# Performance work log

Hardware: AMD Instinct MI355X
Metric: run time of the kernel (lower is better)

## Reference

```python
import jax, jax.numpy as jnp
import numpy as np
from jax import lax

EPS = 1e-5
K = 7
G = 4


def _dwconv_bn(x, w, g, b, m, v):
    # depthwise 3x3, pad 1, then BN (eval mode with running stats)
    C = x.shape[1]
    y = lax.conv_general_dilated(x, w, (1, 1), [(1, 1), (1, 1)],
                                 feature_group_count=C,
                                 dimension_numbers=('NCHW', 'OIHW', 'NCHW'))
    scale = (g / jnp.sqrt(v + EPS))[None, :, None, None]
    return (y - m[None, :, None, None]) * scale + b[None, :, None, None]


def _proj(t, pw1, pb1, pw2, pb2):
    # 1x1 conv -> GELU(exact) -> 1x1 conv, on small spatial maps
    h = jnp.einsum('bchw,oc->bohw', t, pw1) + pb1[None, :, None, None]
    h = jax.nn.gelu(h, approximate=False)
    return jnp.einsum('bchw,oc->bohw', h, pw2) + pb2[None, :, None, None]


def setup_inputs() -> dict:
    key = jax.random.key(0)
    ks = jax.random.split(key, 17)
    B, C, H, W = 16, 256, 56, 56
    r = C // 4
    inp = {
        'x1': jax.random.normal(ks[0], (B, C, H, W), jnp.float32),
        'dw1_w': jax.random.normal(ks[1], (C, 1, 3, 3), jnp.float32) * 0.1,
        'dw1_g': jax.random.uniform(ks[2], (C,), jnp.float32, 0.5, 1.5),
        'dw1_b': jax.random.normal(ks[3], (C,), jnp.float32) * 0.1,
        'dw1_m': jax.random.normal(ks[4], (C,), jnp.float32) * 0.1,
        'dw1_v': jax.random.uniform(ks[5], (C,), jnp.float32, 0.5, 1.5),
        'dw2_w': jax.random.normal(ks[6], (C, 1, 3, 3), jnp.float32) * 0.1,
        'dw2_g': jax.random.uniform(ks[7], (C,), jnp.float32, 0.5, 1.5),
        'dw2_b': jax.random.normal(ks[8], (C,), jnp.float32) * 0.1,
        'dw2_m': jax.random.normal(ks[9], (C,), jnp.float32) * 0.1,
        'dw2_v': jax.random.uniform(ks[10], (C,), jnp.float32, 0.5, 1.5),
        'weight1': jax.random.normal(ks[11], (G, C, K, K), jnp.float32) * 0.02,
        'bias1': jax.random.normal(ks[12], (G, C), jnp.float32) * 0.02,
        'pw1': jax.random.normal(ks[13], (r, C), jnp.float32) * 0.05,
        'pb1': jax.random.normal(ks[14], (r,), jnp.float32) * 0.05,
        'pw2': jax.random.normal(ks[15], (C * G, r), jnp.float32) * 0.05,
        'pb2': jax.random.normal(ks[16], (C * G,), jnp.float32) * 0.05,
    }
    return inp


def reference(x1, dw1_w, dw1_g, dw1_b, dw1_m, dw1_v,
              dw2_w, dw2_g, dw2_b, dw2_m, dw2_v,
              weight1, bias1, pw1, pb1, pw2, pb2):
    B, C, H, W = x1.shape
    # gated fuse: relu6(dw1(x)) * dw2(x)
    a = jnp.clip(_dwconv_bn(x1, dw1_w, dw1_g, dw1_b, dw1_m, dw1_v), 0.0, 6.0)
    x_fuse = a * _dwconv_bn(x1, dw2_w, dw2_g, dw2_b, dw2_m, dw2_v)

    # adaptive avg pool to (K,K): H,W multiples of K -> uniform block means
    pooled = x_fuse.reshape(B, C, K, H // K, K, W // K).mean(axis=(3, 5))

    # dynamic kernel: proj -> softmax over groups -> weighted sum of weight1
    scale1 = _proj(pooled, pw1, pb1, pw2, pb2).reshape(B, G, C, K, K)
    scale1 = jax.nn.softmax(scale1, axis=1)
    w_dyn = jnp.sum(scale1 * weight1[None], axis=1)  # [B, C, K, K]

    # dynamic bias
    mean_x = x_fuse.mean(axis=(-2, -1), keepdims=True)  # [B, C, 1, 1]
    sb = _proj(mean_x, pw1, pb1, pw2, pb2).reshape(B, G, C)
    sb = jax.nn.softmax(sb, axis=1)
    b_dyn = jnp.sum(sb * bias1[None], axis=1)  # [B, C]

    # per-sample depthwise conv with dynamic weights
    pad = K // 2

    def per_sample(xi, wi):  # xi [C,H,W], wi [C,K,K]
        y = lax.conv_general_dilated(xi[None], wi[:, None], (1, 1),
                                     [(pad, pad), (pad, pad)],
                                     feature_group_count=C,
                                     dimension_numbers=('NCHW', 'OIHW', 'NCHW'))
        return y[0]

    out = jax.vmap(per_sample)(x_fuse, w_dyn)  # [B, C, H, W]
    return out + b_dyn[:, :, None, None]
```

## Files before the change

### kernel.cpp

```cpp
#include <hip/hip_runtime.h>
#include <math.h>

#define BATCH 16
#define CH 256
#define HW 56
#define NPIX (HW*HW)

__device__ __forceinline__ void fuse_tile(
    const float* __restrict__ plane, int ty, int tx,
    const float w1[9], const float w2[9],
    float sc1, float be1, float sc2, float be2,
    float res[4][4])
{
    const int oy = 4 * ty;
    float y1a[4][4], y2a[4][4];
    #pragma unroll
    for (int a = 0; a < 4; a++)
        #pragma unroll
        for (int e = 0; e < 4; e++) { y1a[a][e] = 0.f; y2a[a][e] = 0.f; }

    #pragma unroll
    for (int iy = 0; iy < 6; iy++) {
        const int r    = oy - 1 + iy;
        const bool rok = (r >= 0) && (r < 56);
        const int rc   = rok ? r : 0;
        float rb[12];
        #pragma unroll
        for (int k = 0; k < 3; k++) {
            const int cx  = tx - 1 + k;
            const bool cv = (cx >= 0) && (cx < 14);
            const int cc2 = cv ? cx : 0;
            const bool ok = rok && cv;
            float4 v = *(const float4*)(plane + rc*56 + 4*cc2);
            rb[4*k+0] = ok ? v.x : 0.f;
            rb[4*k+1] = ok ? v.y : 0.f;
            rb[4*k+2] = ok ? v.z : 0.f;
            rb[4*k+3] = ok ? v.w : 0.f;
        }
        #pragma unroll
        for (int tyy = 0; tyy < 4; tyy++) {
            const int ky = iy - tyy;
            if (ky >= 0 && ky < 3) {
                #pragma unroll
                for (int e = 0; e < 4; e++)
                    #pragma unroll
                    for (int dj = 0; dj < 3; dj++) {
                        float xv = rb[3 + e + dj];
                        y1a[tyy][e] += xv * w1[ky*3+dj];
                        y2a[tyy][e] += xv * w2[ky*3+dj];
                    }
            }
        }
    }
    #pragma unroll
    for (int tyy = 0; tyy < 4; tyy++)
        #pragma unroll
        for (int e = 0; e < 4; e++) {
            float y1 = y1a[tyy][e] * sc1 + be1;
            float y2 = y2a[tyy][e] * sc2 + be2;
            float a = fminf(fmaxf(y1, 0.f), 6.f);
            res[tyy][e] = a * y2;
        }
}

__global__ __launch_bounds__(256) void k1_pool(
    const float* __restrict__ x1,
    const float* __restrict__ dw1w, const float* __restrict__ g1, const float* __restrict__ b1,
    const float* __restrict__ m1, const float* __restrict__ v1,
    const float* __restrict__ dw2w, const float* __restrict__ g2, const float* __restrict__ b2,
    const float* __restrict__ m2, const float* __restrict__ v2,
    float* __restrict__ pooled)
{
    const int bc = blockIdx.x;
    const int c  = bc & 255;
    const int b  = bc >> 8;
    const int t  = threadIdx.x;

    __shared__ float part[196];

    float w1[9], w2[9];
    #pragma unroll
    for (int k = 0; k < 9; k++) { w1[k] = dw1w[c*9+k]; w2[k] = dw2w[c*9+k]; }
    const float sc1 = g1[c] * rsqrtf(v1[c] + 1e-5f);
    const float be1 = b1[c] - m1[c] * sc1;
    const float sc2 = g2[c] * rsqrtf(v2[c] + 1e-5f);
    const float be2 = b2[c] - m2[c] * sc2;

    if (t < 196) {
        const int ty = t / 14, tx = t - ty * 14;
        float res[4][4];
        fuse_tile(x1 + (size_t)bc * NPIX, ty, tx, w1, w2, sc1, be1, sc2, be2, res);
        float s = 0.f;
        #pragma unroll
        for (int a = 0; a < 4; a++)
            #pragma unroll
            for (int e = 0; e < 4; e++) s += res[a][e];
        part[t] = s;
    }
    __syncthreads();
    if (t < 49) {
        int ph = t / 7, pw = t - ph * 7;
        float s = part[(2*ph  )*14 + 2*pw] + part[(2*ph  )*14 + 2*pw + 1]
                + part[(2*ph+1)*14 + 2*pw] + part[(2*ph+1)*14 + 2*pw + 1];
        pooled[((size_t)(b * 50 + t)) * 256 + c] = s * (1.f/64.f);
    }
}

__global__ __launch_bounds__(256) void k2a(
    const float* __restrict__ pooled,
    const float* __restrict__ pw1, const float* __restrict__ pb1,
    float* __restrict__ h)
{
    const int blk = blockIdx.x;
    const int b = blk / 50, p = blk - b * 50;
    const int t = threadIdx.x;

    __shared__ __attribute__((aligned(16))) float xs[272];

    const float* base = pooled + (size_t)b * 50 * 256;
    float v;
    if (p < 49) {
        v = base[p * 256 + t];
    } else {
        float s = 0.f;
        #pragma unroll 7
        for (int q = 0; q < 49; q++) s += base[q * 256 + t];
        v = s * (1.f/49.f);
    }
    xs[t + 4*(t>>6)] = v;
    __syncthreads();

    const int o = t >> 2, part = t & 3;
    const float4* w4 = (const float4*)(pw1 + o*256 + part*64);
    const float4* x4 = (const float4*)(xs + part*68);
    float acc = 0.f;
    #pragma unroll
    for (int i = 0; i < 16; i++) {
        float4 w = w4[i];
        float4 x = x4[i];
        acc += w.x*x.x + w.y*x.y + w.z*x.z + w.w*x.w;
    }
    acc += __shfl_xor(acc, 1);
    acc += __shfl_xor(acc, 2);
    if (part == 0) {
        float zv = acc + pb1[o];
        h[((size_t)b * 50 + p) * 64 + o] = 0.5f * zv * (1.f + erff(zv * 0.70710678118654752f));
    }
}

__global__ __launch_bounds__(256) void k2b(
    const float* __restrict__ h, const float* __restrict__ pw2, const float* __restrict__ pb2,
    const float* __restrict__ weight1, const float* __restrict__ bias1,
    float* __restrict__ w_dyn,
    float* __restrict__ b_dyn)
{
    const int b   = blockIdx.x;
    const int cch = blockIdx.y;
    const int t   = threadIdx.x;
    const int c_base = cch * 16;

    __shared__ float ht[64*52];
    __shared__ __attribute__((aligned(16))) float wg[16*64*4];

    const float* hp = h + (size_t)b * 50 * 64;
    for (int idx = t; idx < 800; idx += 256) {
        const int p = idx >> 4, k4 = idx & 15;
        float4 v = ((const float4*)(hp + p * 64))[k4];
        ht[(4*k4+0)*52 + p] = v.x;
        ht[(4*k4+1)*52 + p] = v.y;
        ht[(4*k4+2)*52 + p] = v.z;
        ht[(4*k4+3)*52 + p] = v.w;
    }
    for (int idx = t; idx < 1024; idx += 256) {
        const int r = idx >> 4, k4 = idx & 15;
        const int g = r >> 4, cl = r & 15;
        const int o2 = (g << 8) + c_base + cl;
        float4 v = ((const float4*)(pw2 + (size_t)o2 * 64))[k4];
        wg[((cl*64) + 4*k4+0)*4 + g] = v.x;
        wg[((cl*64) + 4*k4+1)*4 + g] = v.y;
        wg[((cl*64) + 4*k4+2)*4 + g] = v.z;
        wg[((cl*64) + 4*k4+3)*4 + g] = v.w;
    }
    __syncthreads();

    for (int idx = t; idx < 800; idx += 256) {
        const int cl = idx / 50, p = idx - cl * 50;
        const int c  = c_base + cl;
        float s0 = pb2[c], s1 = pb2[256 + c], s2 = pb2[512 + c], s3 = pb2[768 + c];
        const float4* wv = (const float4*)wg + cl * 64;
        #pragma unroll
        for (int k = 0; k < 64; k++) {
            const float x = ht[k*52 + p];
            const float4 w = wv[k];
            s0 += x * w.x; s1 += x * w.y; s2 += x * w.z; s3 += x * w.w;
        }
        float mx = fmaxf(fmaxf(s0, s1), fmaxf(s2, s3));
        float e0 = expf(s0-mx), e1 = expf(s1-mx), e2 = expf(s2-mx), e3 = expf(s3-mx);
        float inv = 1.f / (e0+e1+e2+e3);
        e0 *= inv; e1 *= inv; e2 *= inv; e3 *= inv;
        if (p < 49) {
            float wvv = e0*weight1[(0*256+c)*49+p] + e1*weight1[(1*256+c)*49+p]
                      + e2*weight1[(2*256+c)*49+p] + e3*weight1[(3*256+c)*49+p];
            w_dyn[((size_t)b*256 + c)*49 + p] = wvv;
        } else {
            b_dyn[b*256 + c] = e0*bias1[c] + e1*bias1[256+c] + e2*bias1[512+c] + e3*bias1[768+c];
        }
    }
}

#define S3 68
__global__ __launch_bounds__(256) void k3_dyn(
    const float* __restrict__ x1,
    const float* __restrict__ dw1w, const float* __restrict__ g1, const float* __restrict__ b1,
    const float* __restrict__ m1, const float* __restrict__ v1,
    const float* __restrict__ dw2w, const float* __restrict__ g2, const float* __restrict__ b2,
    const float* __restrict__ m2, const float* __restrict__ v2,
    const float* __restrict__ w_dyn, const float* __restrict__ b_dyn,
    float* __restrict__ out)
{
    const int bc = blockIdx.x;
    const int c  = bc & 255;
    const int t  = threadIdx.x;
    __shared__ __attribute__((aligned(16))) float halo[62*S3];

    float w1[9], w2[9];
    #pragma unroll
    for (int k = 0; k < 9; k++) { w1[k] = dw1w[c*9+k]; w2[k] = dw2w[c*9+k]; }
    const float sc1 = g1[c] * rsqrtf(v1[c] + 1e-5f);
    const float be1 = b1[c] - m1[c] * sc1;
    const float sc2 = g2[c] * rsqrtf(v2[c] + 1e-5f);
    const float be2 = b2[c] - m2[c] * sc2;
    float wk[49];
    const float* wp = w_dyn + (size_t)bc * 49;
    #pragma unroll
    for (int k = 0; k < 49; k++) wk[k] = wp[k];
    const float bias = b_dyn[bc];

    {
        float4 z = make_float4(0.f, 0.f, 0.f, 0.f);
        float4* h4 = (float4*)halo;
        for (int i = t; i < 62*S3/4; i += 256) h4[i] = z;
    }
    __syncthreads();

    const int ty = t / 14, tx = t - ty * 14;
    if (t < 196) {
        float res[4][4];
        fuse_tile(x1 + (size_t)bc * NPIX, ty, tx, w1, w2, sc1, be1, sc2, be2, res);
        #pragma unroll
        for (int tyy = 0; tyy < 4; tyy++) {
            float4 r4; r4.x=res[tyy][0]; r4.y=res[tyy][1]; r4.z=res[tyy][2]; r4.w=res[tyy][3];
            *(float4*)&halo[(4*ty + tyy + 3)*S3 + 4 + 4*tx] = r4;
        }
    }
    __syncthreads();

    if (t < 196) {
        const int oy = ty * 4, ox = tx * 4;
        float acc[4][4];
        #pragma unroll
        for (int a = 0; a < 4; a++)
            #pragma unroll
            for (int bb = 0; bb < 4; bb++) acc[a][bb] = bias;

        #pragma unroll
        for (int iy = 0; iy < 10; iy++) {
            const float* hr = &halo[(oy+iy)*S3 + ox];
            float4 a = *(const float4*)hr;
            float4 b = *(const float4*)(hr + 4);
            float4 cc = *(const float4*)(hr + 8);
            float row[12];
            row[0]=a.x; row[1]=a.y; row[2]=a.z; row[3]=a.w;
            row[4]=b.x; row[5]=b.y; row[6]=b.z; row[7]=b.w;
            row[8]=cc.x; row[9]=cc.y; row[10]=cc.z; row[11]=cc.w;
            #pragma unroll
            for (int tyy = 0; tyy < 4; tyy++) {
                const int ky = iy - tyy;
                if (ky >= 0 && ky < 7) {
                    #pragma unroll
                    for (int txx = 0; txx < 4; txx++)
                        #pragma unroll
                        for (int kx = 0; kx < 7; kx++)
                            acc[tyy][txx] += row[1+txx+kx] * wk[ky*7+kx];
                }
            }
        }
        float* op = out + (size_t)bc * NPIX;
        #pragma unroll
        for (int tyy = 0; tyy < 4; tyy++) {
            float4 r4; r4.x = acc[tyy][0]; r4.y = acc[tyy][1]; r4.z = acc[tyy][2]; r4.w = acc[tyy][3];
            *(float4*)(op + (oy+tyy)*56 + ox) = r4;
        }
    }
}

extern "C" void kernel_launch(void* const* d_in, const int* in_sizes, int n_in,
                              void* d_out, int out_size, void* d_ws, size_t ws_size,
                              hipStream_t stream) {
    const float* x1    = (const float*)d_in[0];
    const float* dw1w  = (const float*)d_in[1];
    const float* dw1g  = (const float*)d_in[2];
    const float* dw1b  = (const float*)d_in[3];
    const float* dw1m  = (const float*)d_in[4];
    const float* dw1v  = (const float*)d_in[5];
    const float* dw2w  = (const float*)d_in[6];
    const float* dw2g  = (const float*)d_in[7];
    const float* dw2b  = (const float*)d_in[8];
    const float* dw2m  = (const float*)d_in[9];
    const float* dw2v  = (const float*)d_in[10];
    const float* weight1 = (const float*)d_in[11];
    const float* bias1   = (const float*)d_in[12];
    const float* pw1     = (const float*)d_in[13];
    const float* pb1     = (const float*)d_in[14];
    const float* pw2     = (const float*)d_in[15];
    const float* pb2     = (const float*)d_in[16];

    float* out = (float*)d_out;
    float* ws  = (float*)d_ws;
    float* pooled = ws;
    float* h      = ws + 204800;
    float* w_dyn  = ws + 256000;
    float* b_dyn  = ws + 456704;

    k1_pool<<<BATCH*CH, 256, 0, stream>>>(x1, dw1w, dw1g, dw1b, dw1m, dw1v,
                                          dw2w, dw2g, dw2b, dw2m, dw2v, pooled);
    k2a<<<800, 256, 0, stream>>>(pooled, pw1, pb1, h);
    k2b<<<dim3(BATCH, 16), 256, 0, stream>>>(h, pw2, pb2, weight1, bias1, w_dyn, b_dyn);
    k3_dyn<<<BATCH*CH, 256, 0, stream>>>(x1, dw1w, dw1g, dw1b, dw1m, dw1v,
                                         dw2w, dw2g, dw2b, dw2m, dw2v,
                                         w_dyn, b_dyn, out);
}
```

Measured before the change: 191.9 us.

## Pack dual depthwise FMAs, fuse global mean into pooling, trim halo zeroing

The two 3x3 depthwise convolutions now run as packed two-wide FMAs on float2 vectors, which lets the compiler emit packed FP32 instructions. The global mean used for the dynamic bias is now computed by a wavefront shuffle reduction inside the pooling kernel, so the projection kernel no longer loops over 49 pooled values. In the dynamic-conv kernel, only the halo border of shared memory is zeroed, which removes one __syncthreads and the full-buffer clear. This relies on the interior writes and the border writes never overlapping.

```diff
diff --git a/kernel.cpp b/kernel.cpp
--- a/kernel.cpp
+++ b/kernel.cpp
@@ -6,18 +6,19 @@
 #define HW 56
 #define NPIX (HW*HW)
 
+typedef float f32x2 __attribute__((ext_vector_type(2)));
+
 __device__ __forceinline__ void fuse_tile(
     const float* __restrict__ plane, int ty, int tx,
-    const float w1[9], const float w2[9],
-    float sc1, float be1, float sc2, float be2,
+    const f32x2 w12[9], f32x2 sc12, f32x2 be12,
     float res[4][4])
 {
     const int oy = 4 * ty;
-    float y1a[4][4], y2a[4][4];
+    f32x2 y12a[4][4];
     #pragma unroll
     for (int a = 0; a < 4; a++)
         #pragma unroll
-        for (int e = 0; e < 4; e++) { y1a[a][e] = 0.f; y2a[a][e] = 0.f; }
+        for (int e = 0; e < 4; e++) y12a[a][e] = (f32x2){0.f, 0.f};
 
     #pragma unroll
     for (int iy = 0; iy < 6; iy++) {
@@ -45,9 +46,9 @@
                 for (int e = 0; e < 4; e++)
                     #pragma unroll
                     for (int dj = 0; dj < 3; dj++) {
-                        float xv = rb[3 + e + dj];
-                        y1a[tyy][e] += xv * w1[ky*3+dj];
-                        y2a[tyy][e] += xv * w2[ky*3+dj];
+                        const float xv = rb[3 + e + dj];
+                        const f32x2 xv2 = {xv, xv};
+                        y12a[tyy][e] = __builtin_elementwise_fma(xv2, w12[ky*3+dj], y12a[tyy][e]);
                     }
             }
         }
@@ -56,10 +57,9 @@
     for (int tyy = 0; tyy < 4; tyy++)
         #pragma unroll
         for (int e = 0; e < 4; e++) {
-            float y1 = y1a[tyy][e] * sc1 + be1;
-            float y2 = y2a[tyy][e] * sc2 + be2;
-            float a = fminf(fmaxf(y1, 0.f), 6.f);
-            res[tyy][e] = a * y2;
+            f32x2 yb = __builtin_elementwise_fma(y12a[tyy][e], sc12, be12);
+            float a = fminf(fmaxf(yb.x, 0.f), 6.f);
+            res[tyy][e] = a * yb.y;
         }
 }
 
@@ -78,18 +78,20 @@
 
     __shared__ float part[196];
 
-    float w1[9], w2[9];
-    #pragma unroll
-    for (int k = 0; k < 9; k++) { w1[k] = dw1w[c*9+k]; w2[k] = dw2w[c*9+k]; }
+    f32x2 w12[9];
+    #pragma unroll
+    for (int k = 0; k < 9; k++) w12[k] = (f32x2){dw1w[c*9+k], dw2w[c*9+k]};
     const float sc1 = g1[c] * rsqrtf(v1[c] + 1e-5f);
     const float be1 = b1[c] - m1[c] * sc1;
     const float sc2 = g2[c] * rsqrtf(v2[c] + 1e-5f);
     const float be2 = b2[c] - m2[c] * sc2;
+    const f32x2 sc12 = {sc1, sc2};
+    const f32x2 be12 = {be1, be2};
 
     if (t < 196) {
         const int ty = t / 14, tx = t - ty * 14;
         float res[4][4];
-        fuse_tile(x1 + (size_t)bc * NPIX, ty, tx, w1, w2, sc1, be1, sc2, be2, res);
+        fuse_tile(x1 + (size_t)bc * NPIX, ty, tx, w12, sc12, be12, res);
         float s = 0.f;
         #pragma unroll
         for (int a = 0; a < 4; a++)
@@ -98,11 +100,18 @@
         part[t] = s;
     }
     __syncthreads();
-    if (t < 49) {
-        int ph = t / 7, pw = t - ph * 7;
-        float s = part[(2*ph  )*14 + 2*pw] + part[(2*ph  )*14 + 2*pw + 1]
-                + part[(2*ph+1)*14 + 2*pw] + part[(2*ph+1)*14 + 2*pw + 1];
-        pooled[((size_t)(b * 50 + t)) * 256 + c] = s * (1.f/64.f);
+    if (t < 64) {
+        float cs = 0.f;
+        if (t < 49) {
+            int ph = t / 7, pw = t - ph * 7;
+            cs = part[(2*ph  )*14 + 2*pw] + part[(2*ph  )*14 + 2*pw + 1]
+               + part[(2*ph+1)*14 + 2*pw] + part[(2*ph+1)*14 + 2*pw + 1];
+            pooled[((size_t)(b * 50 + t)) * 256 + c] = cs * (1.f/64.f);
+        }
+        #pragma unroll
+        for (int off = 32; off > 0; off >>= 1) cs += __shfl_down(cs, off);
+        if (t == 0)
+            pooled[((size_t)(b * 50 + 49)) * 256 + c] = cs * (1.f/64.f) * (1.f/49.f);
     }
 }
 
@@ -117,17 +126,7 @@
 
     __shared__ __attribute__((aligned(16))) float xs[272];
 
-    const float* base = pooled + (size_t)b * 50 * 256;
-    float v;
-    if (p < 49) {
-        v = base[p * 256 + t];
-    } else {
-        float s = 0.f;
-        #pragma unroll 7
-        for (int q = 0; q < 49; q++) s += base[q * 256 + t];
-        v = s * (1.f/49.f);
-    }
-    xs[t + 4*(t>>6)] = v;
+    xs[t + 4*(t>>6)] = pooled[((size_t)b * 50 + p) * 256 + t];
     __syncthreads();
 
     const int o = t >> 2, part = t & 3;
@@ -223,30 +222,34 @@
     const int t  = threadIdx.x;
     __shared__ __attribute__((aligned(16))) float halo[62*S3];
 
-    float w1[9], w2[9];
-    #pragma unroll
-    for (int k = 0; k < 9; k++) { w1[k] = dw1w[c*9+k]; w2[k] = dw2w[c*9+k]; }
+    f32x2 w12[9];
+    #pragma unroll
+    for (int k = 0; k < 9; k++) w12[k] = (f32x2){dw1w[c*9+k], dw2w[c*9+k]};
     const float sc1 = g1[c] * rsqrtf(v1[c] + 1e-5f);
     const float be1 = b1[c] - m1[c] * sc1;
     const float sc2 = g2[c] * rsqrtf(v2[c] + 1e-5f);
     const float be2 = b2[c] - m2[c] * sc2;
+    const f32x2 sc12 = {sc1, sc2};
+    const f32x2 be12 = {be1, be2};
     float wk[49];
     const float* wp = w_dyn + (size_t)bc * 49;
     #pragma unroll
     for (int k = 0; k < 49; k++) wk[k] = wp[k];
     const float bias = b_dyn[bc];
 
-    {
-        float4 z = make_float4(0.f, 0.f, 0.f, 0.f);
-        float4* h4 = (float4*)halo;
-        for (int i = t; i < 62*S3/4; i += 256) h4[i] = z;
-    }
-    __syncthreads();
+    if (t < 208) {
+        int row, c4;
+        if (t < 48)       { row = t >> 4;             c4 = t & 15; }
+        else if (t < 96)  { row = 59 + ((t-48) >> 4); c4 = (t-48) & 15; }
+        else if (t < 152) { row = 3 + (t - 96);       c4 = 0; }
+        else              { row = 3 + (t - 152);      c4 = 15; }
+        *(float4*)&halo[row*S3 + 4*c4] = make_float4(0.f, 0.f, 0.f, 0.f);
+    }
 
     const int ty = t / 14, tx = t - ty * 14;
     if (t < 196) {
         float res[4][4];
-        fuse_tile(x1 + (size_t)bc * NPIX, ty, tx, w1, w2, sc1, be1, sc2, be2, res);
+        fuse_tile(x1 + (size_t)bc * NPIX, ty, tx, w12, sc12, be12, res);
         #pragma unroll
         for (int tyy = 0; tyy < 4; tyy++) {
             float4 r4; r4.x=res[tyy][0]; r4.y=res[tyy][1]; r4.z=res[tyy][2]; r4.w=res[tyy][3];
```

Result: no change. 192.2 us (+0.2%).
